# Kernel tuning notes

Measured on AMD Instinct MI355X. Metric: run time of the kernel, lower is better.

The kernel has to match this reference:

```python
import jax, jax.numpy as jnp
import numpy as np

# Static conv hyperparameters (match init_kwargs / setup_inputs)
PAD = 1
DIL = 1
STRIDE_VAL = 2.5          # continuous stride value used in setup_inputs
INT_STRIDE = 2            # floor(STRIDE_VAL): used for output-size arithmetic (static)


def _bilinear_take(x, pos, axis):
    """Linearly interpolate x along `axis` at fractional positions `pos`.

    pos has shape [O, K]; the sampled axis of x is replaced by the two axes
    (O, K). Out-of-range samples contribute zero (deform-conv convention).
    """
    n = x.shape[axis]
    p0 = jnp.floor(pos).astype(jnp.int32)
    frac = (pos - p0.astype(pos.dtype))
    out_shape = x.shape[:axis] + pos.shape + x.shape[axis + 1:]
    bshape = (1,) * axis + pos.shape + (1,) * (x.ndim - axis - 1)

    def take(p):
        valid = ((p >= 0) & (p < n)).astype(x.dtype).reshape(bshape)
        v = jnp.take(x, jnp.clip(p, 0, n - 1).reshape(-1), axis=axis)
        return v.reshape(out_shape) * valid

    w = frac.reshape(bshape).astype(x.dtype)
    return take(p0) * (1.0 - w) + take(p0 + 1) * w


def setup_inputs() -> dict:
    key = jax.random.key(0)
    k1, k2, k3 = jax.random.split(key, 3)
    x = jax.random.normal(k1, (32, 128, 64, 64), dtype=jnp.float32)
    weight = jax.random.normal(k2, (256, 128, 3, 3), dtype=jnp.float32) * 0.05
    bias = jax.random.normal(k3, (256,), dtype=jnp.float32)
    stride_h = jnp.full((1,), STRIDE_VAL, dtype=jnp.float32)
    stride_w = jnp.full((1,), STRIDE_VAL, dtype=jnp.float32)
    return {"x": x, "weight": weight, "bias": bias,
            "stride_h": stride_h, "stride_w": stride_w}


def reference(x, weight, bias, stride_h, stride_w):
    B, C, H, W = x.shape
    O, _, KH, KW = weight.shape
    # output size uses floor(stride), exactly as StrideConv2dFunction._output_size
    OH = (H + 2 * PAD - DIL * (KH - 1) - 1) // INT_STRIDE + 1
    OW = (W + 2 * PAD - DIL * (KW - 1) - 1) // INT_STRIDE + 1
    # fractional im2col sampling positions: out_idx * stride - pad + k * dilation
    pos_h = (jnp.arange(OH, dtype=jnp.float32)[:, None] * stride_h[0]
             - PAD + jnp.arange(KH, dtype=jnp.float32)[None, :] * DIL)  # [OH,KH]
    pos_w = (jnp.arange(OW, dtype=jnp.float32)[:, None] * stride_w[0]
             - PAD + jnp.arange(KW, dtype=jnp.float32)[None, :] * DIL)  # [OW,KW]
    rows = _bilinear_take(x, pos_h, axis=2)          # [B,C,OH,KH,W]
    patches = _bilinear_take(rows, pos_w, axis=4)    # [B,C,OH,KH,OW,KW]
    out = jnp.einsum('bcpkql,ockl->bopq', patches, weight)  # [B,O,OH,OW]
    return out + bias[None, :, None, None]
```

## Files before the change

### kernel.cpp

```cpp
#include <hip/hip_runtime.h>
#include <cstddef>

#define BB  32
#define CC  128
#define HH  64
#define WW  64
#define OO  256
#define OHH 32
#define OWW 32
#define YSTR 196
#define PSTR 296
#define ROWE (32 * YSTR)

typedef __bf16 bf16x8 __attribute__((ext_vector_type(8)));
typedef __bf16 bf16x4 __attribute__((ext_vector_type(4)));
typedef float  f32x4  __attribute__((ext_vector_type(4)));

__global__ void wtrans_bf16_kernel(const float* __restrict__ w, __bf16* __restrict__ wt) {
    int idx = blockIdx.x * 256 + threadIdx.x;
    if (idx >= OO * 9 * CC) return;
    int c    = idx & 127;
    int rest = idx >> 7;
    int k    = rest % 9;
    int o    = rest / 9;
    wt[idx] = (__bf16)w[((size_t)o * CC + c) * 9 + k];
}

__global__ __launch_bounds__(512, 4)
void conv_mfma_kernel(const float* __restrict__ x, const __bf16* __restrict__ wt,
                      const float* __restrict__ bias, const float* __restrict__ shp,
                      const float* __restrict__ swp, float* __restrict__ out) {
    __shared__ __align__(16) __bf16 yrbuf[4 + 2 * ROWE];
    __shared__ __align__(16) __bf16 pT[64 * PSTR];

    const int tid = threadIdx.x;
    const int b   = blockIdx.x;
    const int p0  = blockIdx.y * 2;
    const float sh = shp[0];
    const float sw = swp[0];

    float fh_[2];
    int   hb_[2];
#pragma unroll
    for (int pi = 0; pi < 2; ++pi) {
        float hpos = (float)(p0 + pi) * sh - 1.0f;
        float hbf  = floorf(hpos);
        fh_[pi] = hpos - hbf;
        hb_[pi] = (int)hbf;
    }
    const bool oob0 = (hb_[0] >= HH || hb_[0] <= -4);
    const bool oob1 = (hb_[1] >= HH || hb_[1] <= -4);

    if (oob0 && oob1) {
#pragma unroll
        for (int j = 0; j < 8; ++j) {
            int fi = j * 512 + tid;
            int o  = fi >> 4;
            int rem = fi & 15;
            int pi = rem >> 3;
            int qf = rem & 7;
            float bv = bias[o];
            float4 r; r.x = bv; r.y = bv; r.z = bv; r.w = bv;
            *(float4*)(out + (((size_t)b * OO + o) * OHH + p0 + pi) * OWW + qf * 4) = r;
        }
        return;
    }

    const int piA  = tid >> 8;
    const int t8   = tid & 255;
    const int cA   = t8 >> 3;
    const int colA = (t8 & 7) * 4;
    const float fhA = fh_[piA];
    int  hrA[4];
    bool rvA[4];
#pragma unroll
    for (int r = 0; r < 4; ++r) {
        hrA[r] = hb_[piA] + r;
        rvA[r] = (hrA[r] >= 0) && (hrA[r] < HH);
    }
    __bf16* yrA = yrbuf + 4 + piA * ROWE;

    const int piB = tid >> 8;
    const int qB  = (tid >> 3) & 31;
    const int cB  = (tid & 7) * 4;
    const float wposB = (float)qB * sw - 1.0f;
    const float wbfB  = floorf(wposB);
    const float fw    = wposB - wbfB;
    const int   wbq   = (int)wbfB;
    const int   wba   = min(wbq & ~3, 60);
    const int   e     = wbq - wba;
    const bool  g1 = e >= 1, g2 = e >= 2, g3 = e >= 3;
    bool mv[4];
#pragma unroll
    for (int j = 0; j < 4; ++j) mv[j] = ((unsigned)(wbq + j) < (unsigned)WW);
    const __bf16* yrB = yrbuf + 4 + piB * ROWE;

    const int wv = tid >> 6;
    const int l  = tid & 63;
    const int lr = l & 15;
    const int lg = l >> 4;
    const int o0 = wv * 32;

    f32x4 acc[2][4];
#pragma unroll
    for (int ot = 0; ot < 2; ++ot)
#pragma unroll
        for (int nt = 0; nt < 4; ++nt) acc[ot][nt] = (f32x4)0.0f;

    if (tid < 4) yrbuf[tid] = (__bf16)0.0f;

    for (int chunk = 0; chunk < 4; ++chunk) {
        const int c0 = chunk * 32;

        {
            const float* xp = x + ((size_t)(b * CC + c0 + cA) * HH) * WW;
            float4 v0[4], v1[4];
#pragma unroll
            for (int r = 0; r < 4; ++r) {
                float4 t0 = {0.f, 0.f, 0.f, 0.f}, t1 = t0;
                if (rvA[r]) {
                    const float* rp = xp + (size_t)hrA[r] * WW;
                    t0 = *(const float4*)(rp + colA);
                    t1 = *(const float4*)(rp + colA + 32);
                }
                v0[r] = t0; v1[r] = t1;
            }
            __bf16* yw = yrA + cA * YSTR;
#pragma unroll
            for (int kh = 0; kh < 3; ++kh) {
                bf16x4 ta, tb;
                ta[0] = (__bf16)(v0[kh].x + fhA * (v0[kh + 1].x - v0[kh].x));
                ta[1] = (__bf16)(v0[kh].y + fhA * (v0[kh + 1].y - v0[kh].y));
                ta[2] = (__bf16)(v0[kh].z + fhA * (v0[kh + 1].z - v0[kh].z));
                ta[3] = (__bf16)(v0[kh].w + fhA * (v0[kh + 1].w - v0[kh].w));
                tb[0] = (__bf16)(v1[kh].x + fhA * (v1[kh + 1].x - v1[kh].x));
                tb[1] = (__bf16)(v1[kh].y + fhA * (v1[kh + 1].y - v1[kh].y));
                tb[2] = (__bf16)(v1[kh].z + fhA * (v1[kh + 1].z - v1[kh].z));
                tb[3] = (__bf16)(v1[kh].w + fhA * (v1[kh + 1].w - v1[kh].w));
                *(bf16x4*)(yw + kh * 64 + colA)      = ta;
                *(bf16x4*)(yw + kh * 64 + colA + 32) = tb;
            }
        }
        __syncthreads();

        {
            __bf16* pq = &pT[(piB * 32 + qB) * PSTR + cB];
            float tv[3][3][4];
#pragma unroll
            for (int ci = 0; ci < 4; ++ci) {
                const __bf16* yc = yrB + (cB + ci) * YSTR + wba;
#pragma unroll
                for (int kh = 0; kh < 3; ++kh) {
                    bf16x4 a  = *(const bf16x4*)(yc + kh * 64);
                    bf16x4 bq = *(const bf16x4*)(yc + kh * 64 + 4);
                    float v0 = (float)a[0], v1 = (float)a[1], v2 = (float)a[2], v3 = (float)a[3];
                    float v4 = (float)bq[0], v5 = (float)bq[1], v6 = (float)bq[2];
                    float s0 = g1 ? v1 : v0; s0 = g2 ? v2 : s0; s0 = g3 ? v3 : s0;
                    float s1 = g1 ? v2 : v1; s1 = g2 ? v3 : s1; s1 = g3 ? v4 : s1;
                    float s2 = g1 ? v3 : v2; s2 = g2 ? v4 : s2; s2 = g3 ? v5 : s2;
                    float s3 = g1 ? v4 : v3; s3 = g2 ? v5 : s3; s3 = g3 ? v6 : s3;
                    s0 = mv[0] ? s0 : 0.0f;
                    s1 = mv[1] ? s1 : 0.0f;
                    s2 = mv[2] ? s2 : 0.0f;
                    s3 = mv[3] ? s3 : 0.0f;
                    tv[kh][0][ci] = s0 + fw * (s1 - s0);
                    tv[kh][1][ci] = s1 + fw * (s2 - s1);
                    tv[kh][2][ci] = s2 + fw * (s3 - s2);
                }
            }
#pragma unroll
            for (int kh = 0; kh < 3; ++kh)
#pragma unroll
                for (int kw = 0; kw < 3; ++kw) {
                    bf16x4 pr;
                    pr[0] = (__bf16)tv[kh][kw][0];
                    pr[1] = (__bf16)tv[kh][kw][1];
                    pr[2] = (__bf16)tv[kh][kw][2];
                    pr[3] = (__bf16)tv[kh][kw][3];
                    *(bf16x4*)(pq + (kh * 3 + kw) * 32) = pr;
                }
        }
        __syncthreads();

        __builtin_amdgcn_s_setprio(1);
#pragma unroll
        for (int k = 0; k < 9; ++k) {
            const __bf16* wp = wt + ((size_t)(o0 + lr) * 9 + k) * CC + c0 + lg * 8;
            bf16x8 a0 = *(const bf16x8*)(wp);
            bf16x8 a1 = *(const bf16x8*)(wp + (size_t)16 * 9 * CC);
            bf16x8 b0 = *(const bf16x8*)&pT[(0  + lr) * PSTR + k * 32 + lg * 8];
            bf16x8 b1 = *(const bf16x8*)&pT[(16 + lr) * PSTR + k * 32 + lg * 8];
            bf16x8 b2 = *(const bf16x8*)&pT[(32 + lr) * PSTR + k * 32 + lg * 8];
            bf16x8 b3 = *(const bf16x8*)&pT[(48 + lr) * PSTR + k * 32 + lg * 8];
            acc[0][0] = __builtin_amdgcn_mfma_f32_16x16x32_bf16(a0, b0, acc[0][0], 0, 0, 0);
            acc[0][1] = __builtin_amdgcn_mfma_f32_16x16x32_bf16(a0, b1, acc[0][1], 0, 0, 0);
            acc[0][2] = __builtin_amdgcn_mfma_f32_16x16x32_bf16(a0, b2, acc[0][2], 0, 0, 0);
            acc[0][3] = __builtin_amdgcn_mfma_f32_16x16x32_bf16(a0, b3, acc[0][3], 0, 0, 0);
            acc[1][0] = __builtin_amdgcn_mfma_f32_16x16x32_bf16(a1, b0, acc[1][0], 0, 0, 0);
            acc[1][1] = __builtin_amdgcn_mfma_f32_16x16x32_bf16(a1, b1, acc[1][1], 0, 0, 0);
            acc[1][2] = __builtin_amdgcn_mfma_f32_16x16x32_bf16(a1, b2, acc[1][2], 0, 0, 0);
            acc[1][3] = __builtin_amdgcn_mfma_f32_16x16x32_bf16(a1, b3, acc[1][3], 0, 0, 0);
        }
        __builtin_amdgcn_s_setprio(0);
    }

#pragma unroll
    for (int ot = 0; ot < 2; ++ot) {
#pragma unroll
        for (int r = 0; r < 4; ++r) {
            int o = o0 + ot * 16 + lg * 4 + r;
            float bv = bias[o];
#pragma unroll
            for (int nt = 0; nt < 4; ++nt) {
                int pi = nt >> 1;
                int qc = (nt & 1) * 16 + lr;
                out[(((size_t)b * OO + o) * OHH + p0 + pi) * OWW + qc] = acc[ot][nt][r] + bv;
            }
        }
    }
}

__global__ __launch_bounds__(256)
void conv_fallback_kernel(const float* __restrict__ x, const float* __restrict__ w,
                          const float* __restrict__ bias, const float* __restrict__ shp,
                          const float* __restrict__ swp, float* __restrict__ out) {
    __shared__ __align__(16) float xr[4][WW];
    __shared__ __align__(16) float patch[9][OWW];
    const int tid = threadIdx.x;
    const int p = blockIdx.y;
    const int b = blockIdx.x;
    const float sh = shp[0];
    const float sw = swp[0];
    const float hpos = (float)p * sh - 1.0f;
    const float hbf  = floorf(hpos);
    const float fh   = hpos - hbf;
    const int   hb   = (int)hbf;
    const int og = tid & 63;
    const int qg = tid >> 6;
    const int o0 = og * 4;
    const int q0 = qg * 8;
    const int rr   = tid >> 6;
    const int colc = tid & 63;
    const int rowg = hb + rr;
    const bool rv = (rowg >= 0) && (rowg < HH);
    float acc[4][8];
#pragma unroll
    for (int i = 0; i < 4; ++i)
#pragma unroll
        for (int j = 0; j < 8; ++j) acc[i][j] = 0.0f;
    for (int c = 0; c < CC; ++c) {
        float vv = 0.0f;
        if (rv) vv = x[(((size_t)b * CC + c) * HH + rowg) * WW + colc];
        xr[rr][colc] = vv;
        __syncthreads();
        for (int it = tid; it < 9 * OWW; it += 256) {
            int k = it >> 5; int q = it & 31;
            int kh = k / 3;  int kw = k - kh * 3;
            float wpos = (float)q * sw - 1.0f + (float)kw;
            float wbf = floorf(wpos);
            float fw = wpos - wbf;
            int wb = (int)wbf;
            float x00 = 0, x01 = 0, x10 = 0, x11 = 0;
            if (wb >= 0 && wb < WW)         { x00 = xr[kh][wb];     x10 = xr[kh + 1][wb]; }
            if (wb + 1 >= 0 && wb + 1 < WW) { x01 = xr[kh][wb + 1]; x11 = xr[kh + 1][wb + 1]; }
            float top = x00 * (1.0f - fw) + x01 * fw;
            float bot = x10 * (1.0f - fw) + x11 * fw;
            patch[k][q] = top * (1.0f - fh) + bot * fh;
        }
        __syncthreads();
        const float4* pv = (const float4*)&patch[0][0];
#pragma unroll
        for (int k = 0; k < 9; ++k) {
            const float* wb_ = w + (size_t)o0 * (CC * 9) + c * 9 + k;
            float wvv[4] = {wb_[0], wb_[1 * CC * 9], wb_[2 * CC * 9], wb_[3 * CC * 9]};
            float4 pa = pv[k * 8 + (q0 >> 2)];
            float4 pb = pv[k * 8 + (q0 >> 2) + 1];
#pragma unroll
            for (int oo2 = 0; oo2 < 4; ++oo2) {
                acc[oo2][0] += wvv[oo2] * pa.x; acc[oo2][1] += wvv[oo2] * pa.y;
                acc[oo2][2] += wvv[oo2] * pa.z; acc[oo2][3] += wvv[oo2] * pa.w;
                acc[oo2][4] += wvv[oo2] * pb.x; acc[oo2][5] += wvv[oo2] * pb.y;
                acc[oo2][6] += wvv[oo2] * pb.z; acc[oo2][7] += wvv[oo2] * pb.w;
            }
        }
    }
    float4 bv = ((const float4*)bias)[og];
    float bvv[4] = {bv.x, bv.y, bv.z, bv.w};
#pragma unroll
    for (int oo2 = 0; oo2 < 4; ++oo2) {
        size_t off = (((size_t)b * OO + o0 + oo2) * OHH + p) * OWW + q0;
        float4 r0, r1;
        r0.x = acc[oo2][0] + bvv[oo2]; r0.y = acc[oo2][1] + bvv[oo2];
        r0.z = acc[oo2][2] + bvv[oo2]; r0.w = acc[oo2][3] + bvv[oo2];
        r1.x = acc[oo2][4] + bvv[oo2]; r1.y = acc[oo2][5] + bvv[oo2];
        r1.z = acc[oo2][6] + bvv[oo2]; r1.w = acc[oo2][7] + bvv[oo2];
        *(float4*)(out + off)     = r0;
        *(float4*)(out + off + 4) = r1;
    }
}

extern "C" void kernel_launch(void* const* d_in, const int* in_sizes, int n_in,
                              void* d_out, int out_size, void* d_ws, size_t ws_size,
                              hipStream_t stream) {
    const float* x    = (const float*)d_in[0];
    const float* w    = (const float*)d_in[1];
    const float* bias = (const float*)d_in[2];
    const float* shp  = (const float*)d_in[3];
    const float* swp  = (const float*)d_in[4];
    float* out = (float*)d_out;

    const size_t wt_bytes = (size_t)OO * 9 * CC * sizeof(__bf16);
    if (ws_size >= wt_bytes) {
        __bf16* wtp = (__bf16*)d_ws;
        int n = OO * 9 * CC;
        wtrans_bf16_kernel<<<(n + 255) / 256, 256, 0, stream>>>(w, wtp);
        dim3 grid(BB, OHH / 2);
        conv_mfma_kernel<<<grid, 512, 0, stream>>>(x, wtp, bias, shp, swp, out);
    } else {
        dim3 grid(BB, OHH);
        conv_fallback_kernel<<<grid, 256, 0, stream>>>(x, w, bias, shp, swp, out);
    }
}
```

Baseline: 55.28 us.

## Retile MFMA warp work to 64 outputs x 32 positions and reorganize patch LDS layout

Each wave now computes 64 output channels by 32 spatial positions (4x2 MFMA tiles) instead of 32 by 64, with waves split into channel groups and output-row halves. The patch buffer in shared memory is relaid out tap-major with 16-position tiles, so each B-fragment read is a contiguous, unpadded block. This halves LDS fragment reads per MFMA and doubles global weight fragment loads, trading LDS traffic for more global/L2 traffic. The layout change also removes the padded stride, so bank conflicts may change.

```diff
diff --git a/kernel.cpp b/kernel.cpp
--- a/kernel.cpp
+++ b/kernel.cpp
@@ -9,8 +9,9 @@
 #define OHH 32
 #define OWW 32
 #define YSTR 196
-#define PSTR 296
 #define ROWE (32 * YSTR)
+#define PT_TAP 2048
+#define PT_QT  512
 
 typedef __bf16 bf16x8 __attribute__((ext_vector_type(8)));
 typedef __bf16 bf16x4 __attribute__((ext_vector_type(4)));
@@ -31,7 +32,7 @@
                       const float* __restrict__ bias, const float* __restrict__ shp,
                       const float* __restrict__ swp, float* __restrict__ out) {
     __shared__ __align__(16) __bf16 yrbuf[4 + 2 * ROWE];
-    __shared__ __align__(16) __bf16 pT[64 * PSTR];
+    __shared__ __align__(16) __bf16 pT[9 * PT_TAP];
 
     const int tid = threadIdx.x;
     const int b   = blockIdx.x;
@@ -94,18 +95,24 @@
 #pragma unroll
     for (int j = 0; j < 4; ++j) mv[j] = ((unsigned)(wbq + j) < (unsigned)WW);
     const __bf16* yrB = yrbuf + 4 + piB * ROWE;
+    const int qg_ = piB * 32 + qB;
+    const int qt_ = qg_ >> 4;
+    const int qr_ = qg_ & 15;
+    __bf16* pqBase = pT + qt_ * PT_QT + qr_ * 32 + (cB >> 3) * 8 + (cB & 7);
 
     const int wv = tid >> 6;
     const int l  = tid & 63;
     const int lr = l & 15;
     const int lg = l >> 4;
-    const int o0 = wv * 32;
-
-    f32x4 acc[2][4];
-#pragma unroll
-    for (int ot = 0; ot < 2; ++ot)
-#pragma unroll
-        for (int nt = 0; nt < 4; ++nt) acc[ot][nt] = (f32x4)0.0f;
+    const int og = wv >> 1;
+    const int qh = wv & 1;
+    const int o0 = og * 64;
+
+    f32x4 acc[4][2];
+#pragma unroll
+    for (int ot = 0; ot < 4; ++ot)
+#pragma unroll
+        for (int nt = 0; nt < 2; ++nt) acc[ot][nt] = (f32x4)0.0f;
 
     if (tid < 4) yrbuf[tid] = (__bf16)0.0f;
 
@@ -144,7 +151,6 @@
         __syncthreads();
 
         {
-            __bf16* pq = &pT[(piB * 32 + qB) * PSTR + cB];
             float tv[3][3][4];
 #pragma unroll
             for (int ci = 0; ci < 4; ++ci) {
@@ -177,7 +183,7 @@
                     pr[1] = (__bf16)tv[kh][kw][1];
                     pr[2] = (__bf16)tv[kh][kw][2];
                     pr[3] = (__bf16)tv[kh][kw][3];
-                    *(bf16x4*)(pq + (kh * 3 + kw) * 32) = pr;
+                    *(bf16x4*)(pqBase + (kh * 3 + kw) * PT_TAP) = pr;
                 }
         }
         __syncthreads();
@@ -188,33 +194,34 @@
             const __bf16* wp = wt + ((size_t)(o0 + lr) * 9 + k) * CC + c0 + lg * 8;
             bf16x8 a0 = *(const bf16x8*)(wp);
             bf16x8 a1 = *(const bf16x8*)(wp + (size_t)16 * 9 * CC);
-            bf16x8 b0 = *(const bf16x8*)&pT[(0  + lr) * PSTR + k * 32 + lg * 8];
-            bf16x8 b1 = *(const bf16x8*)&pT[(16 + lr) * PSTR + k * 32 + lg * 8];
-            bf16x8 b2 = *(const bf16x8*)&pT[(32 + lr) * PSTR + k * 32 + lg * 8];
-            bf16x8 b3 = *(const bf16x8*)&pT[(48 + lr) * PSTR + k * 32 + lg * 8];
+            bf16x8 a2 = *(const bf16x8*)(wp + (size_t)32 * 9 * CC);
+            bf16x8 a3 = *(const bf16x8*)(wp + (size_t)48 * 9 * CC);
+            const __bf16* pb = pT + k * PT_TAP + (qh * 2) * PT_QT + lr * 32 + lg * 8;
+            bf16x8 b0 = *(const bf16x8*)(pb);
+            bf16x8 b1 = *(const bf16x8*)(pb + PT_QT);
             acc[0][0] = __builtin_amdgcn_mfma_f32_16x16x32_bf16(a0, b0, acc[0][0], 0, 0, 0);
             acc[0][1] = __builtin_amdgcn_mfma_f32_16x16x32_bf16(a0, b1, acc[0][1], 0, 0, 0);
-            acc[0][2] = __builtin_amdgcn_mfma_f32_16x16x32_bf16(a0, b2, acc[0][2], 0, 0, 0);
-            acc[0][3] = __builtin_amdgcn_mfma_f32_16x16x32_bf16(a0, b3, acc[0][3], 0, 0, 0);
             acc[1][0] = __builtin_amdgcn_mfma_f32_16x16x32_bf16(a1, b0, acc[1][0], 0, 0, 0);
             acc[1][1] = __builtin_amdgcn_mfma_f32_16x16x32_bf16(a1, b1, acc[1][1], 0, 0, 0);
-            acc[1][2] = __builtin_amdgcn_mfma_f32_16x16x32_bf16(a1, b2, acc[1][2], 0, 0, 0);
-            acc[1][3] = __builtin_amdgcn_mfma_f32_16x16x32_bf16(a1, b3, acc[1][3], 0, 0, 0);
+            acc[2][0] = __builtin_amdgcn_mfma_f32_16x16x32_bf16(a2, b0, acc[2][0], 0, 0, 0);
+            acc[2][1] = __builtin_amdgcn_mfma_f32_16x16x32_bf16(a2, b1, acc[2][1], 0, 0, 0);
+            acc[3][0] = __builtin_amdgcn_mfma_f32_16x16x32_bf16(a3, b0, acc[3][0], 0, 0, 0);
+            acc[3][1] = __builtin_amdgcn_mfma_f32_16x16x32_bf16(a3, b1, acc[3][1], 0, 0, 0);
         }
         __builtin_amdgcn_s_setprio(0);
     }
 
-#pragma unroll
-    for (int ot = 0; ot < 2; ++ot) {
-#pragma unroll
-        for (int r = 0; r < 4; ++r) {
-            int o = o0 + ot * 16 + lg * 4 + r;
-            float bv = bias[o];
-#pragma unroll
-            for (int nt = 0; nt < 4; ++nt) {
-                int pi = nt >> 1;
-                int qc = (nt & 1) * 16 + lr;
-                out[(((size_t)b * OO + o) * OHH + p0 + pi) * OWW + qc] = acc[ot][nt][r] + bv;
+    {
+        const int p = p0 + qh;
+#pragma unroll
+        for (int ot = 0; ot < 4; ++ot) {
+#pragma unroll
+            for (int r = 0; r < 4; ++r) {
+                int o = o0 + ot * 16 + lg * 4 + r;
+                float bv = bias[o];
+                float* op = out + (((size_t)b * OO + o) * OHH + p) * OWW;
+                op[lr]      = acc[ot][0][r] + bv;
+                op[16 + lr] = acc[ot][1][r] + bv;
             }
         }
     }
```

Result: slower. 86.34 us (+56.2%).

## Process four output rows per block to double weight reuse per MFMA tile

Applied to the files above, without the earlier changes.

Each block now computes four output rows instead of two, doubling the N dimension of its MFMA tile. Every weight fragment loaded from global memory is reused across eight B tiles instead of four, and the grid shrinks by half. The cost is double the LDS use per block, more accumulator registers (launch bounds lowered to 2 blocks per SM), and fewer blocks in flight, which cuts occupancy and latency hiding.

```diff
diff --git a/kernel.cpp b/kernel.cpp
--- a/kernel.cpp
+++ b/kernel.cpp
@@ -26,37 +26,37 @@
     wt[idx] = (__bf16)w[((size_t)o * CC + c) * 9 + k];
 }
 
-__global__ __launch_bounds__(512, 4)
+__global__ __launch_bounds__(512, 2)
 void conv_mfma_kernel(const float* __restrict__ x, const __bf16* __restrict__ wt,
                       const float* __restrict__ bias, const float* __restrict__ shp,
                       const float* __restrict__ swp, float* __restrict__ out) {
-    __shared__ __align__(16) __bf16 yrbuf[4 + 2 * ROWE];
-    __shared__ __align__(16) __bf16 pT[64 * PSTR];
+    __shared__ __align__(16) __bf16 yrbuf[4 + 4 * ROWE];
+    __shared__ __align__(16) __bf16 pT[128 * PSTR];
 
     const int tid = threadIdx.x;
     const int b   = blockIdx.x;
-    const int p0  = blockIdx.y * 2;
+    const int p0  = blockIdx.y * 4;
     const float sh = shp[0];
     const float sw = swp[0];
 
-    float fh_[2];
-    int   hb_[2];
-#pragma unroll
-    for (int pi = 0; pi < 2; ++pi) {
+    float fh_[4];
+    int   hb_[4];
+    bool  oob[4];
+#pragma unroll
+    for (int pi = 0; pi < 4; ++pi) {
         float hpos = (float)(p0 + pi) * sh - 1.0f;
         float hbf  = floorf(hpos);
         fh_[pi] = hpos - hbf;
         hb_[pi] = (int)hbf;
-    }
-    const bool oob0 = (hb_[0] >= HH || hb_[0] <= -4);
-    const bool oob1 = (hb_[1] >= HH || hb_[1] <= -4);
-
-    if (oob0 && oob1) {
-#pragma unroll
-        for (int j = 0; j < 8; ++j) {
+        oob[pi] = (hb_[pi] >= HH || hb_[pi] <= -4);
+    }
+
+    if (oob[0] && oob[1] && oob[2] && oob[3]) {
+#pragma unroll
+        for (int j = 0; j < 16; ++j) {
             int fi = j * 512 + tid;
-            int o  = fi >> 4;
-            int rem = fi & 15;
+            int o  = fi >> 5;
+            int rem = fi & 31;
             int pi = rem >> 3;
             int qf = rem & 7;
             float bv = bias[o];
@@ -66,10 +66,10 @@
         return;
     }
 
-    const int piA  = tid >> 8;
-    const int t8   = tid & 255;
-    const int cA   = t8 >> 3;
-    const int colA = (t8 & 7) * 4;
+    const int piA = tid >> 7;
+    const int t7  = tid & 127;
+    const int cA  = t7 >> 2;
+    const int cg0 = (t7 & 3) * 16;
     const float fhA = fh_[piA];
     int  hrA[4];
     bool rvA[4];
@@ -80,9 +80,9 @@
     }
     __bf16* yrA = yrbuf + 4 + piA * ROWE;
 
-    const int piB = tid >> 8;
-    const int qB  = (tid >> 3) & 31;
-    const int cB  = (tid & 7) * 4;
+    const int piB = tid >> 7;
+    const int qB  = (tid >> 2) & 31;
+    const int cB  = (tid & 3) * 8;
     const float wposB = (float)qB * sw - 1.0f;
     const float wbfB  = floorf(wposB);
     const float fw    = wposB - wbfB;
@@ -94,6 +94,7 @@
 #pragma unroll
     for (int j = 0; j < 4; ++j) mv[j] = ((unsigned)(wbq + j) < (unsigned)WW);
     const __bf16* yrB = yrbuf + 4 + piB * ROWE;
+    __bf16* pqRow = pT + (piB * 32 + qB) * PSTR;
 
     const int wv = tid >> 6;
     const int l  = tid & 63;
@@ -101,11 +102,11 @@
     const int lg = l >> 4;
     const int o0 = wv * 32;
 
-    f32x4 acc[2][4];
+    f32x4 acc[2][8];
 #pragma unroll
     for (int ot = 0; ot < 2; ++ot)
 #pragma unroll
-        for (int nt = 0; nt < 4; ++nt) acc[ot][nt] = (f32x4)0.0f;
+        for (int nt = 0; nt < 8; ++nt) acc[ot][nt] = (f32x4)0.0f;
 
     if (tid < 4) yrbuf[tid] = (__bf16)0.0f;
 
@@ -114,41 +115,41 @@
 
         {
             const float* xp = x + ((size_t)(b * CC + c0 + cA) * HH) * WW;
-            float4 v0[4], v1[4];
+            float4 v[4][4];
 #pragma unroll
             for (int r = 0; r < 4; ++r) {
-                float4 t0 = {0.f, 0.f, 0.f, 0.f}, t1 = t0;
                 if (rvA[r]) {
-                    const float* rp = xp + (size_t)hrA[r] * WW;
-                    t0 = *(const float4*)(rp + colA);
-                    t1 = *(const float4*)(rp + colA + 32);
+                    const float* rp = xp + (size_t)hrA[r] * WW + cg0;
+#pragma unroll
+                    for (int g = 0; g < 4; ++g) v[r][g] = *(const float4*)(rp + g * 4);
+                } else {
+#pragma unroll
+                    for (int g = 0; g < 4; ++g) { v[r][g].x = 0.f; v[r][g].y = 0.f; v[r][g].z = 0.f; v[r][g].w = 0.f; }
                 }
-                v0[r] = t0; v1[r] = t1;
-            }
-            __bf16* yw = yrA + cA * YSTR;
+            }
+            __bf16* yw = yrA + cA * YSTR + cg0;
 #pragma unroll
             for (int kh = 0; kh < 3; ++kh) {
-                bf16x4 ta, tb;
-                ta[0] = (__bf16)(v0[kh].x + fhA * (v0[kh + 1].x - v0[kh].x));
-                ta[1] = (__bf16)(v0[kh].y + fhA * (v0[kh + 1].y - v0[kh].y));
-                ta[2] = (__bf16)(v0[kh].z + fhA * (v0[kh + 1].z - v0[kh].z));
-                ta[3] = (__bf16)(v0[kh].w + fhA * (v0[kh + 1].w - v0[kh].w));
-                tb[0] = (__bf16)(v1[kh].x + fhA * (v1[kh + 1].x - v1[kh].x));
-                tb[1] = (__bf16)(v1[kh].y + fhA * (v1[kh + 1].y - v1[kh].y));
-                tb[2] = (__bf16)(v1[kh].z + fhA * (v1[kh + 1].z - v1[kh].z));
-                tb[3] = (__bf16)(v1[kh].w + fhA * (v1[kh + 1].w - v1[kh].w));
-                *(bf16x4*)(yw + kh * 64 + colA)      = ta;
-                *(bf16x4*)(yw + kh * 64 + colA + 32) = tb;
+#pragma unroll
+                for (int g = 0; g < 4; ++g) {
+                    bf16x4 t;
+                    t[0] = (__bf16)(v[kh][g].x + fhA * (v[kh + 1][g].x - v[kh][g].x));
+                    t[1] = (__bf16)(v[kh][g].y + fhA * (v[kh + 1][g].y - v[kh][g].y));
+                    t[2] = (__bf16)(v[kh][g].z + fhA * (v[kh + 1][g].z - v[kh][g].z));
+                    t[3] = (__bf16)(v[kh][g].w + fhA * (v[kh + 1][g].w - v[kh][g].w));
+                    *(bf16x4*)(yw + kh * 64 + g * 4) = t;
+                }
             }
         }
         __syncthreads();
 
-        {
-            __bf16* pq = &pT[(piB * 32 + qB) * PSTR + cB];
+#pragma unroll
+        for (int g = 0; g < 2; ++g) {
+            const int cc0 = cB + g * 4;
             float tv[3][3][4];
 #pragma unroll
             for (int ci = 0; ci < 4; ++ci) {
-                const __bf16* yc = yrB + (cB + ci) * YSTR + wba;
+                const __bf16* yc = yrB + (cc0 + ci) * YSTR + wba;
 #pragma unroll
                 for (int kh = 0; kh < 3; ++kh) {
                     bf16x4 a  = *(const bf16x4*)(yc + kh * 64);
@@ -177,7 +178,7 @@
                     pr[1] = (__bf16)tv[kh][kw][1];
                     pr[2] = (__bf16)tv[kh][kw][2];
                     pr[3] = (__bf16)tv[kh][kw][3];
-                    *(bf16x4*)(pq + (kh * 3 + kw) * 32) = pr;
+                    *(bf16x4*)(pqRow + (kh * 3 + kw) * 32 + cc0) = pr;
                 }
         }
         __syncthreads();
@@ -188,18 +189,15 @@
             const __bf16* wp = wt + ((size_t)(o0 + lr) * 9 + k) * CC + c0 + lg * 8;
             bf16x8 a0 = *(const bf16x8*)(wp);
             bf16x8 a1 = *(const bf16x8*)(wp + (size_t)16 * 9 * CC);
-            bf16x8 b0 = *(const bf16x8*)&pT[(0  + lr) * PSTR + k * 32 + lg * 8];
-            bf16x8 b1 = *(const bf16x8*)&pT[(16 + lr) * PSTR + k * 32 + lg * 8];
-            bf16x8 b2 = *(const bf16x8*)&pT[(32 + lr) * PSTR + k * 32 + lg * 8];
-            bf16x8 b3 = *(const bf16x8*)&pT[(48 + lr) * PSTR + k * 32 + lg * 8];
-            acc[0][0] = __builtin_amdgcn_mfma_f32_16x16x32_bf16(a0, b0, acc[0][0], 0, 0, 0);
-            acc[0][1] = __builtin_amdgcn_mfma_f32_16x16x32_bf16(a0, b1, acc[0][1], 0, 0, 0);
-            acc[0][2] = __builtin_amdgcn_mfma_f32_16x16x32_bf16(a0, b2, acc[0][2], 0, 0, 0);
-            acc[0][3] = __builtin_amdgcn_mfma_f32_16x16x32_bf16(a0, b3, acc[0][3], 0, 0, 0);
-            acc[1][0] = __builtin_amdgcn_mfma_f32_16x16x32_bf16(a1, b0, acc[1][0], 0, 0, 0);
-            acc[1][1] = __builtin_amdgcn_mfma_f32_16x16x32_bf16(a1, b1, acc[1][1], 0, 0, 0);
-            acc[1][2] = __builtin_amdgcn_mfma_f32_16x16x32_bf16(a1, b2, acc[1][2], 0, 0, 0);
-            acc[1][3] = __builtin_amdgcn_mfma_f32_16x16x32_bf16(a1, b3, acc[1][3], 0, 0, 0);
+            bf16x8 bfr[8];
+#pragma unroll
+            for (int nt = 0; nt < 8; ++nt)
+                bfr[nt] = *(const bf16x8*)&pT[(nt * 16 + lr) * PSTR + k * 32 + lg * 8];
+#pragma unroll
+            for (int nt = 0; nt < 8; ++nt) {
+                acc[0][nt] = __builtin_amdgcn_mfma_f32_16x16x32_bf16(a0, bfr[nt], acc[0][nt], 0, 0, 0);
+                acc[1][nt] = __builtin_amdgcn_mfma_f32_16x16x32_bf16(a1, bfr[nt], acc[1][nt], 0, 0, 0);
+            }
         }
         __builtin_amdgcn_s_setprio(0);
     }
@@ -211,7 +209,7 @@
             int o = o0 + ot * 16 + lg * 4 + r;
             float bv = bias[o];
 #pragma unroll
-            for (int nt = 0; nt < 4; ++nt) {
+            for (int nt = 0; nt < 8; ++nt) {
                 int pi = nt >> 1;
                 int qc = (nt & 1) * 16 + lr;
                 out[(((size_t)b * OO + o) * OHH + p0 + pi) * OWW + qc] = acc[ot][nt][r] + bv;
@@ -314,7 +312,7 @@
         __bf16* wtp = (__bf16*)d_ws;
         int n = OO * 9 * CC;
         wtrans_bf16_kernel<<<(n + 255) / 256, 256, 0, stream>>>(w, wtp);
-        dim3 grid(BB, OHH / 2);
+        dim3 grid(BB, OHH / 4);
         conv_mfma_kernel<<<grid, 512, 0, stream>>>(x, wtp, bias, shp, swp, out);
     } else {
         dim3 grid(BB, OHH);
```

After: 55.08 us. About the same (-0.4%).
